# Optimization experiments

Hardware: AMD Instinct MI355X
Metric: run time of the kernel (lower is better)

## Reference

```python
import jax, jax.numpy as jnp
import numpy as np

B, L, D = 8, 30, 512
NS, NI = 21, 8  # n_slot_caps = n_slots+1, n_intent_caps = n_intents+1


def setup_inputs() -> dict:
    key = jax.random.key(0)
    ks = jax.random.split(key, 6)
    s = 0.02  # keep pose magnitudes sane
    return {
        "token_features": jax.random.normal(ks[0], (B, L, D), jnp.float32),
        "cls_token": jax.random.normal(ks[1], (B, D), jnp.float32),
        "w_route_ws": jax.random.normal(ks[2], (L, NS, D), jnp.float32) * s,
        "w_pose_ws": jax.random.normal(ks[3], (L, NS, D, D), jnp.float32) * s,
        "w_route_si": jax.random.normal(ks[4], (NS, NI, D), jnp.float32) * s,
        "w_pose_si": jax.random.normal(ks[5], (NS, NI, D, D), jnp.float32) * s,
    }


def reference(token_features, cls_token, w_route_ws, w_pose_ws, w_route_si, w_pose_si):
    d_model = token_features.shape[-1]
    # ---- route words -> slots ----
    a_words = token_features.sum(-1) / d_model                      # (b, l)
    c_ws = jax.nn.softmax(
        jnp.einsum('lnj,blj->bln', w_route_ws, token_features), axis=-1)  # (b, l, n_slot)
    wc = c_ws * a_words[:, :, None]                                 # (b, l, n_slot)
    weighted_c = wc.sum(axis=1)                                     # (b, n_slot)
    a_slots = weighted_c / a_words.sum(-1, keepdims=True)           # (b, n_slot)
    u_hat_slots = jnp.einsum('lnij,blj->blni', w_pose_ws, token_features)  # (b, l, n_slot, d)
    u_slots = jnp.einsum('bls,blsk->bsk', wc, u_hat_slots) / weighted_c[:, :, None]
    slots = jnp.argmax(c_ws, axis=-1)                               # (b, l)
    # ---- route slots -> intents ----
    c_si = jax.nn.softmax(
        jnp.einsum('sij,bsj->bsi', w_route_si, u_slots), axis=-1)   # (b, n_slot, n_int)
    wc2 = c_si * a_slots[:, :, None]                                # (b, n_slot, n_int)
    weighted_c2 = wc2.sum(axis=1)                                   # (b, n_int)
    a_intents = weighted_c2 / a_slots.sum(-1, keepdims=True)        # (b, n_int)
    u_hat_intents = jnp.einsum('sijk,bsk->bsik', w_pose_si, u_slots)  # (b, n_slot, n_int, d)
    u_intents = jnp.einsum('bsi,bsik->bik', wc2, u_hat_intents) / weighted_c2[:, :, None]
    # ---- argmax dispatch + cls residual ----
    max_idx = jnp.argmax(a_intents, axis=-1)                        # (b,)
    poses = jnp.take_along_axis(u_intents, max_idx[:, None, None], axis=1)[:, 0, :]
    intents = cls_token + poses                                     # (b, d)
    return (slots, intents)
```

## Files before the change

kernel.cpp:

```cpp
#include <hip/hip_runtime.h>

#define B 8
#define L 30
#define D 512
#define NS 21
#define NI 8

__device__ __forceinline__ float block_reduce_sum_256(float v, float* red) {
  int lane = threadIdx.x & 63;
  int wid  = threadIdx.x >> 6;
  #pragma unroll
  for (int o = 32; o > 0; o >>= 1) v += __shfl_down(v, o, 64);
  __syncthreads();
  if (lane == 0) red[wid] = v;
  __syncthreads();
  float r = 0.f;
  if (threadIdx.x == 0) {
    #pragma unroll
    for (int w = 0; w < 4; w++) r += red[w];
  }
  return r;
}

__global__ void k_phase_a(const float* __restrict__ x,
                          const float* __restrict__ w_route_ws,
                          float* __restrict__ wc,
                          float* __restrict__ a_words,
                          float* __restrict__ slots_out) {
  __shared__ float red[4];
  __shared__ float logits[NS];
  __shared__ float s_aw;
  int bl = blockIdx.x;
  int l  = bl % L;
  const float* xv = x + (size_t)bl * D;

  float p = 0.f;
  for (int j = threadIdx.x; j < D; j += 256) p += xv[j];
  float tot = block_reduce_sum_256(p, red);
  if (threadIdx.x == 0) { s_aw = tot / (float)D; a_words[bl] = s_aw; }

  for (int n = 0; n < NS; n++) {
    const float* wr = w_route_ws + (size_t)(l * NS + n) * D;
    float q = 0.f;
    for (int j = threadIdx.x; j < D; j += 256) q += wr[j] * xv[j];
    float t = block_reduce_sum_256(q, red);
    if (threadIdx.x == 0) logits[n] = t;
  }
  __syncthreads();
  if (threadIdx.x == 0) {
    float m = logits[0]; int am = 0;
    #pragma unroll
    for (int n = 1; n < NS; n++) if (logits[n] > m) { m = logits[n]; am = n; }
    float e[NS]; float se = 0.f;
    #pragma unroll
    for (int n = 0; n < NS; n++) { e[n] = __expf(logits[n] - m); se += e[n]; }
    float sc = s_aw / se;
    #pragma unroll
    for (int n = 0; n < NS; n++) wc[(size_t)bl * NS + n] = e[n] * sc;
    slots_out[bl] = (float)am;
  }
}

__global__ void k_stats1(const float* __restrict__ wc,
                         const float* __restrict__ a_words,
                         float* __restrict__ weighted_c,
                         float* __restrict__ a_slots) {
  __shared__ float aw_sum[B];
  int t = threadIdx.x;
  if (t < B) {
    float s = 0.f;
    for (int l = 0; l < L; l++) s += a_words[t * L + l];
    aw_sum[t] = s;
  }
  __syncthreads();
  if (t < B * NS) {
    int b = t / NS, n = t % NS;
    float s = 0.f;
    for (int l = 0; l < L; l++) s += wc[(size_t)(b * L + l) * NS + n];
    weighted_c[t] = s;
    a_slots[t] = s / aw_sum[b];
  }
}

__global__ void __launch_bounds__(256) k_u_slots(
    const float* __restrict__ x,
    const float* __restrict__ w_pose_ws,
    const float* __restrict__ wc,
    const float* __restrict__ weighted_c,
    float* __restrict__ u_slots) {
  __shared__ float lwc[B * L];
  __shared__ float lwcn[B];
  int n     = blockIdx.x >> 5;
  int itile = blockIdx.x & 31;
  int wave  = threadIdx.x >> 6;
  int lane  = threadIdx.x & 63;
  int i0    = itile * 16 + wave * 4;

  if (threadIdx.x < B * L) lwc[threadIdx.x] = wc[(size_t)threadIdx.x * NS + n];
  if (threadIdx.x >= 240 && threadIdx.x < 240 + B)
    lwcn[threadIdx.x - 240] = weighted_c[(threadIdx.x - 240) * NS + n];
  __syncthreads();

  float acc[4][B];
  #pragma unroll
  for (int r = 0; r < 4; r++)
    #pragma unroll
    for (int b = 0; b < B; b++) acc[r][b] = 0.f;

  for (int l = 0; l < L; l++) {
    const float* wrow = w_pose_ws + ((size_t)(l * NS + n) * D + i0) * D;
    float4 w0[4], w1[4];
    #pragma unroll
    for (int r = 0; r < 4; r++) {
      const float4* wp = (const float4*)(wrow + (size_t)r * D) + lane * 2;
      w0[r] = wp[0]; w1[r] = wp[1];
    }
    #pragma unroll
    for (int b = 0; b < B; b++) {
      const float4* xp = (const float4*)(x + (size_t)(b * L + l) * D) + lane * 2;
      float4 x0 = xp[0], x1 = xp[1];
      float wcl = lwc[b * L + l];
      #pragma unroll
      for (int r = 0; r < 4; r++) {
        float t = w0[r].x * x0.x + w0[r].y * x0.y + w0[r].z * x0.z + w0[r].w * x0.w
                + w1[r].x * x1.x + w1[r].y * x1.y + w1[r].z * x1.z + w1[r].w * x1.w;
        acc[r][b] += wcl * t;
      }
    }
  }
  #pragma unroll
  for (int r = 0; r < 4; r++)
    #pragma unroll
    for (int b = 0; b < B; b++)
      #pragma unroll
      for (int o = 32; o > 0; o >>= 1) acc[r][b] += __shfl_xor(acc[r][b], o, 64);
  if (lane == 0) {
    #pragma unroll
    for (int r = 0; r < 4; r++)
      #pragma unroll
      for (int b = 0; b < B; b++)
        u_slots[((size_t)b * NS + n) * D + (i0 + r)] = acc[r][b] / lwcn[b];
  }
}

__global__ void k_route_si(const float* __restrict__ u_slots,
                           const float* __restrict__ w_route_si,
                           const float* __restrict__ a_slots,
                           float* __restrict__ wc2) {
  __shared__ float red[4];
  __shared__ float logits[NI];
  int bs = blockIdx.x;
  int s  = bs % NS;
  const float* uv = u_slots + (size_t)bs * D;
  for (int i = 0; i < NI; i++) {
    const float* wr = w_route_si + (size_t)(s * NI + i) * D;
    float q = 0.f;
    for (int j = threadIdx.x; j < D; j += 256) q += wr[j] * uv[j];
    float t = block_reduce_sum_256(q, red);
    if (threadIdx.x == 0) logits[i] = t;
  }
  __syncthreads();
  if (threadIdx.x == 0) {
    float m = logits[0];
    #pragma unroll
    for (int i = 1; i < NI; i++) m = fmaxf(m, logits[i]);
    float e[NI]; float se = 0.f;
    #pragma unroll
    for (int i = 0; i < NI; i++) { e[i] = __expf(logits[i] - m); se += e[i]; }
    float sc = a_slots[bs] / se;
    #pragma unroll
    for (int i = 0; i < NI; i++) wc2[(size_t)bs * NI + i] = e[i] * sc;
  }
}

__global__ void k_stats2(const float* __restrict__ wc2,
                         const float* __restrict__ a_slots,
                         float* __restrict__ weighted_c2,
                         int* __restrict__ max_idx) {
  __shared__ float asum[B];
  __shared__ float ai[B * NI];
  int t = threadIdx.x;
  if (t < B) {
    float s = 0.f;
    for (int n = 0; n < NS; n++) s += a_slots[t * NS + n];
    asum[t] = s;
  }
  float w = 0.f;
  if (t < B * NI) {
    int b = t / NI, i = t % NI;
    for (int ss = 0; ss < NS; ss++) w += wc2[(size_t)(b * NS + ss) * NI + i];
    weighted_c2[t] = w;
  }
  __syncthreads();
  if (t < B * NI) ai[t] = w / asum[t / NI];
  __syncthreads();
  if (t < B) {
    float m = ai[t * NI]; int am = 0;
    #pragma unroll
    for (int i = 1; i < NI; i++) { float v = ai[t * NI + i]; if (v > m) { m = v; am = i; } }
    max_idx[t] = am;
  }
}

__global__ void k_pose_si(const float* __restrict__ w_pose_si,
                          const float* __restrict__ u_slots,
                          const float* __restrict__ wc2,
                          const int* __restrict__ max_idx,
                          float* __restrict__ poses) {
  const int JS = 4;
  int idx = blockIdx.x;
  int b   = idx / (NS * JS);
  int rem = idx - b * (NS * JS);
  int s   = rem / JS, jc = rem % JS;
  int i   = max_idx[b];
  int k   = threadIdx.x;
  const float* wb = w_pose_si + (size_t)(s * NI + i) * D * D + k;
  float cs = 0.f;
  int j0 = jc * (D / JS);
  #pragma unroll 8
  for (int j = j0; j < j0 + D / JS; j++) cs += wb[(size_t)j * D];
  float val = wc2[(size_t)(b * NS + s) * NI + i] *
              u_slots[(size_t)(b * NS + s) * D + k] * cs;
  atomicAdd(&poses[b * D + k], val);
}

__global__ void k_final(const float* __restrict__ cls,
                        const float* __restrict__ poses,
                        const float* __restrict__ weighted_c2,
                        const int* __restrict__ max_idx,
                        float* __restrict__ out_intents) {
  int b = blockIdx.x, k = threadIdx.x;
  out_intents[b * D + k] =
      cls[b * D + k] + poses[b * D + k] / weighted_c2[b * NI + max_idx[b]];
}

extern "C" void kernel_launch(void* const* d_in, const int* in_sizes, int n_in,
                              void* d_out, int out_size, void* d_ws, size_t ws_size,
                              hipStream_t stream) {
  const float* x    = (const float*)d_in[0];
  const float* cls  = (const float*)d_in[1];
  const float* wrws = (const float*)d_in[2];
  const float* wpws = (const float*)d_in[3];
  const float* wrsi = (const float*)d_in[4];
  const float* wpsi = (const float*)d_in[5];

  float* out         = (float*)d_out;
  float* slots_out   = out;
  float* intents_out = out + B * L;

  float* wsf         = (float*)d_ws;
  float* wc          = wsf;
  float* a_words     = wc + B * L * NS;
  float* weighted_c  = a_words + B * L;
  float* a_slots     = weighted_c + B * NS;
  float* u_slots     = a_slots + B * NS;
  float* wc2         = u_slots + B * NS * D;
  float* weighted_c2 = wc2 + B * NS * NI;
  float* poses       = weighted_c2 + B * NI;
  int*   max_idx     = (int*)(poses + B * D);

  hipMemsetAsync(poses, 0, B * D * sizeof(float), stream);
  k_phase_a<<<B * L, 256, 0, stream>>>(x, wrws, wc, a_words, slots_out);
  k_stats1<<<1, 256, 0, stream>>>(wc, a_words, weighted_c, a_slots);
  k_u_slots<<<NS * 32, 256, 0, stream>>>(x, wpws, wc, weighted_c, u_slots);
  k_route_si<<<B * NS, 256, 0, stream>>>(u_slots, wrsi, a_slots, wc2);
  k_stats2<<<1, 256, 0, stream>>>(wc2, a_slots, weighted_c2, max_idx);
  k_pose_si<<<B * NS * 4, 512, 0, stream>>>(wpsi, u_slots, wc2, max_idx, poses);
  k_final<<<B, 512, 0, stream>>>(cls, poses, weighted_c2, max_idx, intents_out);
}
```

Measured before the change: 1.036 ms.

## Use per-wave dot products, finer u_slots tiling, fold memset into stats2

The block-wide reductions in the word and slot routing kernels are replaced by one wave per output row with float4 loads and shuffle-xor reductions. This removes repeated __syncthreads barriers. The u_slots kernel now gives each wave a single output row instead of four, which quadruples the grid to expose more parallelism and cut register use, at the cost of reloading x more often. The memset of poses is moved into k_stats2 to drop one separate stream operation.

```diff
diff --git a/kernel.cpp b/kernel.cpp
--- a/kernel.cpp
+++ b/kernel.cpp
@@ -6,20 +6,15 @@
 #define NS 21
 #define NI 8
 
-__device__ __forceinline__ float block_reduce_sum_256(float v, float* red) {
-  int lane = threadIdx.x & 63;
-  int wid  = threadIdx.x >> 6;
+__device__ __forceinline__ float dot8(float4 a0, float4 a1, float4 b0, float4 b1) {
+  return a0.x * b0.x + a0.y * b0.y + a0.z * b0.z + a0.w * b0.w +
+         a1.x * b1.x + a1.y * b1.y + a1.z * b1.z + a1.w * b1.w;
+}
+
+__device__ __forceinline__ float wave_reduce(float q) {
   #pragma unroll
-  for (int o = 32; o > 0; o >>= 1) v += __shfl_down(v, o, 64);
-  __syncthreads();
-  if (lane == 0) red[wid] = v;
-  __syncthreads();
-  float r = 0.f;
-  if (threadIdx.x == 0) {
-    #pragma unroll
-    for (int w = 0; w < 4; w++) r += red[w];
-  }
-  return r;
+  for (int o = 32; o > 0; o >>= 1) q += __shfl_xor(q, o, 64);
+  return q;
 }
 
 __global__ void k_phase_a(const float* __restrict__ x,
@@ -27,27 +22,32 @@
                           float* __restrict__ wc,
                           float* __restrict__ a_words,
                           float* __restrict__ slots_out) {
-  __shared__ float red[4];
   __shared__ float logits[NS];
   __shared__ float s_aw;
-  int bl = blockIdx.x;
-  int l  = bl % L;
-  const float* xv = x + (size_t)bl * D;
-
-  float p = 0.f;
-  for (int j = threadIdx.x; j < D; j += 256) p += xv[j];
-  float tot = block_reduce_sum_256(p, red);
-  if (threadIdx.x == 0) { s_aw = tot / (float)D; a_words[bl] = s_aw; }
-
-  for (int n = 0; n < NS; n++) {
-    const float* wr = w_route_ws + (size_t)(l * NS + n) * D;
-    float q = 0.f;
-    for (int j = threadIdx.x; j < D; j += 256) q += wr[j] * xv[j];
-    float t = block_reduce_sum_256(q, red);
-    if (threadIdx.x == 0) logits[n] = t;
+  int bl   = blockIdx.x;
+  int l    = bl % L;
+  int wave = threadIdx.x >> 6;
+  int lane = threadIdx.x & 63;
+  const float4* xv = (const float4*)(x + (size_t)bl * D) + lane * 2;
+  float4 x0 = xv[0], x1 = xv[1];
+
+  for (int r = wave; r < NS + 1; r += 4) {
+    float q;
+    if (r < NS) {
+      const float4* wr = (const float4*)(w_route_ws + (size_t)(l * NS + r) * D) + lane * 2;
+      q = dot8(wr[0], wr[1], x0, x1);
+    } else {
+      q = x0.x + x0.y + x0.z + x0.w + x1.x + x1.y + x1.z + x1.w;
+    }
+    q = wave_reduce(q);
+    if (lane == 0) {
+      if (r < NS) logits[r] = q;
+      else        s_aw = q / (float)D;
+    }
   }
   __syncthreads();
   if (threadIdx.x == 0) {
+    a_words[bl] = s_aw;
     float m = logits[0]; int am = 0;
     #pragma unroll
     for (int n = 1; n < NS; n++) if (logits[n] > m) { m = logits[n]; am = n; }
@@ -90,56 +90,37 @@
     float* __restrict__ u_slots) {
   __shared__ float lwc[B * L];
   __shared__ float lwcn[B];
-  int n     = blockIdx.x >> 5;
-  int itile = blockIdx.x & 31;
+  int n     = blockIdx.x >> 7;
+  int itile = blockIdx.x & 127;
   int wave  = threadIdx.x >> 6;
   int lane  = threadIdx.x & 63;
-  int i0    = itile * 16 + wave * 4;
+  int i     = itile * 4 + wave;
 
   if (threadIdx.x < B * L) lwc[threadIdx.x] = wc[(size_t)threadIdx.x * NS + n];
   if (threadIdx.x >= 240 && threadIdx.x < 240 + B)
     lwcn[threadIdx.x - 240] = weighted_c[(threadIdx.x - 240) * NS + n];
   __syncthreads();
 
-  float acc[4][B];
+  float acc[B];
   #pragma unroll
-  for (int r = 0; r < 4; r++)
-    #pragma unroll
-    for (int b = 0; b < B; b++) acc[r][b] = 0.f;
+  for (int b = 0; b < B; b++) acc[b] = 0.f;
 
   for (int l = 0; l < L; l++) {
-    const float* wrow = w_pose_ws + ((size_t)(l * NS + n) * D + i0) * D;
-    float4 w0[4], w1[4];
-    #pragma unroll
-    for (int r = 0; r < 4; r++) {
-      const float4* wp = (const float4*)(wrow + (size_t)r * D) + lane * 2;
-      w0[r] = wp[0]; w1[r] = wp[1];
-    }
+    const float4* wp = (const float4*)(w_pose_ws + ((size_t)(l * NS + n) * D + i) * D) + lane * 2;
+    float4 w0 = wp[0], w1 = wp[1];
     #pragma unroll
     for (int b = 0; b < B; b++) {
       const float4* xp = (const float4*)(x + (size_t)(b * L + l) * D) + lane * 2;
       float4 x0 = xp[0], x1 = xp[1];
-      float wcl = lwc[b * L + l];
-      #pragma unroll
-      for (int r = 0; r < 4; r++) {
-        float t = w0[r].x * x0.x + w0[r].y * x0.y + w0[r].z * x0.z + w0[r].w * x0.w
-                + w1[r].x * x1.x + w1[r].y * x1.y + w1[r].z * x1.z + w1[r].w * x1.w;
-        acc[r][b] += wcl * t;
-      }
+      acc[b] += lwc[b * L + l] * dot8(w0, w1, x0, x1);
     }
   }
   #pragma unroll
-  for (int r = 0; r < 4; r++)
+  for (int b = 0; b < B; b++) acc[b] = wave_reduce(acc[b]);
+  if (lane == 0) {
     #pragma unroll
     for (int b = 0; b < B; b++)
-      #pragma unroll
-      for (int o = 32; o > 0; o >>= 1) acc[r][b] += __shfl_xor(acc[r][b], o, 64);
-  if (lane == 0) {
-    #pragma unroll
-    for (int r = 0; r < 4; r++)
-      #pragma unroll
-      for (int b = 0; b < B; b++)
-        u_slots[((size_t)b * NS + n) * D + (i0 + r)] = acc[r][b] / lwcn[b];
+      u_slots[((size_t)b * NS + n) * D + i] = acc[b] / lwcn[b];
   }
 }
 
@@ -147,17 +128,18 @@
                            const float* __restrict__ w_route_si,
                            const float* __restrict__ a_slots,
                            float* __restrict__ wc2) {
-  __shared__ float red[4];
   __shared__ float logits[NI];
-  int bs = blockIdx.x;
-  int s  = bs % NS;
-  const float* uv = u_slots + (size_t)bs * D;
-  for (int i = 0; i < NI; i++) {
-    const float* wr = w_route_si + (size_t)(s * NI + i) * D;
-    float q = 0.f;
-    for (int j = threadIdx.x; j < D; j += 256) q += wr[j] * uv[j];
-    float t = block_reduce_sum_256(q, red);
-    if (threadIdx.x == 0) logits[i] = t;
+  int bs   = blockIdx.x;
+  int s    = bs % NS;
+  int wave = threadIdx.x >> 6;
+  int lane = threadIdx.x & 63;
+  const float4* uv = (const float4*)(u_slots + (size_t)bs * D) + lane * 2;
+  float4 u0 = uv[0], u1 = uv[1];
+  for (int i = wave; i < NI; i += 4) {
+    const float4* wr = (const float4*)(w_route_si + (size_t)(s * NI + i) * D) + lane * 2;
+    float q = dot8(wr[0], wr[1], u0, u1);
+    q = wave_reduce(q);
+    if (lane == 0) logits[i] = q;
   }
   __syncthreads();
   if (threadIdx.x == 0) {
@@ -176,10 +158,12 @@
 __global__ void k_stats2(const float* __restrict__ wc2,
                          const float* __restrict__ a_slots,
                          float* __restrict__ weighted_c2,
-                         int* __restrict__ max_idx) {
+                         int* __restrict__ max_idx,
+                         float* __restrict__ poses) {
   __shared__ float asum[B];
   __shared__ float ai[B * NI];
   int t = threadIdx.x;
+  for (int idx = t; idx < B * D; idx += 256) poses[idx] = 0.f;
   if (t < B) {
     float s = 0.f;
     for (int n = 0; n < NS; n++) s += a_slots[t * NS + n];
@@ -259,12 +243,11 @@
   float* poses       = weighted_c2 + B * NI;
   int*   max_idx     = (int*)(poses + B * D);
 
-  hipMemsetAsync(poses, 0, B * D * sizeof(float), stream);
   k_phase_a<<<B * L, 256, 0, stream>>>(x, wrws, wc, a_words, slots_out);
   k_stats1<<<1, 256, 0, stream>>>(wc, a_words, weighted_c, a_slots);
-  k_u_slots<<<NS * 32, 256, 0, stream>>>(x, wpws, wc, weighted_c, u_slots);
+  k_u_slots<<<NS * 128, 256, 0, stream>>>(x, wpws, wc, weighted_c, u_slots);
   k_route_si<<<B * NS, 256, 0, stream>>>(u_slots, wrsi, a_slots, wc2);
-  k_stats2<<<1, 256, 0, stream>>>(wc2, a_slots, weighted_c2, max_idx);
+  k_stats2<<<1, 256, 0, stream>>>(wc2, a_slots, weighted_c2, max_idx, poses);
   k_pose_si<<<B * NS * 4, 512, 0, stream>>>(wpsi, u_slots, wc2, max_idx, poses);
   k_final<<<B, 512, 0, stream>>>(cls, poses, weighted_c2, max_idx, intents_out);
 }
```

After: 1.175 ms. 13.4% more time.
